# Kernel optimization log

Hardware: AMD Instinct MI355X
Metric: run time of the kernel (lower is better)

Reference implementation:

```python
import jax, jax.numpy as jnp
import numpy as np

B, S, D, H = 2, 2048, 2048, 16
HD = D // H  # head dim = 128

def setup_inputs() -> dict:
    key = jax.random.key(0)
    ks = jax.random.split(key, 5)
    x = jax.random.normal(ks[0], (B, S, D), dtype=jnp.float32)
    # causal mask: True means block that position (per docstring)
    mask = jnp.triu(jnp.ones((S, S), dtype=bool), k=1)
    scale = 1.0 / np.sqrt(D)
    Wq = jax.random.normal(ks[1], (D, D), dtype=jnp.float32) * scale
    Wk = jax.random.normal(ks[2], (D, D), dtype=jnp.float32) * scale
    Wv = jax.random.normal(ks[3], (D, D), dtype=jnp.float32) * scale
    Wo = jax.random.normal(ks[4], (D, D), dtype=jnp.float32) * scale
    return {"x": x, "mask": mask, "Wq": Wq, "Wk": Wk, "Wv": Wv, "Wo": Wo}

def _split_heads(t):
    b, s, _ = t.shape
    return t.reshape(b, s, H, HD).transpose(0, 2, 1, 3)  # (b, h, s, hd)

def reference(x, mask, Wq, Wk, Wv, Wo):
    # nn.Linear(bias=False): y = x @ W.T
    q = _split_heads(x @ Wq.T)
    k = _split_heads(x @ Wk.T)
    v = _split_heads(x @ Wv.T)
    scale = HD ** -0.5
    scores = jnp.einsum('bhqd,bhkd->bhqk', q, k) * scale  # (b,h,s,s)
    scores = jnp.where(mask[None, None, :, :], -jnp.inf, scores)
    weights = jax.nn.softmax(scores, axis=-1)  # dropout is identity at eval
    out = jnp.einsum('bhqk,bhkd->bhqd', weights, v)
    out = out.transpose(0, 2, 1, 3).reshape(x.shape[0], x.shape[1], D)
    return out @ Wo.T
```

## Files before the change

kernel.cpp:

```cpp
#include <hip/hip_runtime.h>
#include <hip/hip_bf16.h>

typedef __bf16 bf16x8 __attribute__((ext_vector_type(8)));
typedef float f32x4 __attribute__((ext_vector_type(4)));
typedef unsigned short ushort8v __attribute__((ext_vector_type(8)));

__device__ __forceinline__ unsigned short f2bf(float f) {
    unsigned int u = __float_as_uint(f);
    u = (u + 0x7fffu + ((u >> 16) & 1u)) >> 16;
    return (unsigned short)u;
}

__device__ __forceinline__ f32x4 mfma16(bf16x8 a, bf16x8 b, f32x4 c) {
    return __builtin_amdgcn_mfma_f32_16x16x32_bf16(a, b, c, 0, 0, 0);
}

__device__ __forceinline__ void store_c(unsigned short* p, float v) { *p = f2bf(v); }
__device__ __forceinline__ void store_c(float* p, float v) { *p = v; }

__global__ __launch_bounds__(256) void cast_f32_bf16(const float* __restrict__ in,
                                                     unsigned short* __restrict__ out,
                                                     int n4) {
    int i = blockIdx.x * blockDim.x + threadIdx.x;
    if (i < n4) {
        float4 f = ((const float4*)in)[i];
        ushort4 u;
        u.x = f2bf(f.x); u.y = f2bf(f.y); u.z = f2bf(f.z); u.w = f2bf(f.w);
        ((ushort4*)out)[i] = u;
    }
}

__global__ __launch_bounds__(256) void transpose_v(const unsigned short* __restrict__ v,
                                                   unsigned short* __restrict__ vt) {
    __shared__ unsigned short t[64][65];
    const int tid = threadIdx.x;
    const int s0 = blockIdx.x * 64;
    const int d0 = blockIdx.y * 64;
    const int bh = blockIdx.z;
    const int b = bh >> 4, h = bh & 15;

#pragma unroll
    for (int i = 0; i < 2; ++i) {
        int idx = i * 256 + tid;
        int r = idx >> 3, c8 = (idx & 7) * 8;
        ushort8v d = *(const ushort8v*)(v + ((size_t)(b * 2048 + s0 + r)) * 2048 + h * 128 + d0 + c8);
#pragma unroll
        for (int j = 0; j < 8; ++j) t[r][c8 + j] = d[j];
    }
    __syncthreads();
#pragma unroll
    for (int i = 0; i < 2; ++i) {
        int idx = i * 256 + tid;
        int dr = idx >> 3, sc8 = (idx & 7) * 8;
        ushort8v o;
#pragma unroll
        for (int j = 0; j < 8; ++j) o[j] = t[sc8 + j][dr];
        *(ushort8v*)(vt + ((size_t)(bh * 128 + d0 + dr)) * 2048 + s0 + sc8) = o;
    }
}

__device__ __forceinline__ void stage_tile(const unsigned short* __restrict__ A,
                                           const unsigned short* __restrict__ B,
                                           char* lAslot, char* lBslot,
                                           int row0, int col0, int kt, int K,
                                           int tid, int w) {
#pragma unroll
    for (int j = 0; j < 2; ++j) {
        int ci = j * 512 + tid;
        int r = ci >> 2, p = ci & 3;
        int c = p ^ ((r >> 1) & 3);
        size_t goff = ((size_t)(row0 + r) * K + kt + c * 8) * 2;
        __builtin_amdgcn_global_load_lds(
            (__attribute__((address_space(1))) void*)(void*)((const char*)A + goff),
            (__attribute__((address_space(3))) void*)(lAslot + (j * 512 + w * 64) * 16),
            16, 0, 0);
    }
    {
        int ci = tid;
        int r = ci >> 2, p = ci & 3;
        int c = p ^ ((r >> 1) & 3);
        size_t goff = ((size_t)(col0 + r) * K + kt + c * 8) * 2;
        __builtin_amdgcn_global_load_lds(
            (__attribute__((address_space(1))) void*)(void*)((const char*)B + goff),
            (__attribute__((address_space(3))) void*)(lBslot + (w * 64) * 16),
            16, 0, 0);
    }
}

template <typename OUT_T>
__global__ __launch_bounds__(512) void gemm_bt2(const unsigned short* __restrict__ A,
                                                const unsigned short* __restrict__ B,
                                                OUT_T* __restrict__ C,
                                                int M, int N, int K) {
    __shared__ __align__(16) unsigned short lA[3][256 * 32];
    __shared__ __align__(16) unsigned short lB[3][128 * 32];

    const int tid = threadIdx.x;
    const int w = tid >> 6, lane = tid & 63;
    const int wm = w >> 2, wn = w & 3;
    const int lane16 = lane & 15, g = lane >> 4;
    const int row0 = blockIdx.y * 256, col0 = blockIdx.x * 128;
    const int NT = K >> 5;

    f32x4 acc[8][2] = {};

    stage_tile(A, B, (char*)lA[0], (char*)lB[0], row0, col0, 0, K, tid, w);
    stage_tile(A, B, (char*)lA[1], (char*)lB[1], row0, col0, 32, K, tid, w);
    stage_tile(A, B, (char*)lA[2], (char*)lB[2], row0, col0, 64, K, tid, w);

    int s = 0;
#pragma unroll 1
    for (int t = 0; t < NT; ++t) {
        if (t + 2 < NT)      asm volatile("s_waitcnt vmcnt(6)" ::: "memory");
        else if (t + 1 < NT) asm volatile("s_waitcnt vmcnt(3)" ::: "memory");
        else                 asm volatile("s_waitcnt vmcnt(0)" ::: "memory");
        __builtin_amdgcn_s_barrier();
        asm volatile("" ::: "memory");

        bf16x8 aF[8], bF[2];
#pragma unroll
        for (int mf = 0; mf < 8; ++mf) {
            int r = wm * 128 + mf * 16 + lane16;
            aF[mf] = *(const bf16x8*)&lA[s][r * 32 + (g ^ ((r >> 1) & 3)) * 8];
        }
#pragma unroll
        for (int nf = 0; nf < 2; ++nf) {
            int r = wn * 32 + nf * 16 + lane16;
            bF[nf] = *(const bf16x8*)&lB[s][r * 32 + (g ^ ((r >> 1) & 3)) * 8];
        }
        __builtin_amdgcn_s_setprio(1);
#pragma unroll
        for (int mf = 0; mf < 8; ++mf)
#pragma unroll
            for (int nf = 0; nf < 2; ++nf)
                acc[mf][nf] = mfma16(aF[mf], bF[nf], acc[mf][nf]);
        __builtin_amdgcn_s_setprio(0);

        asm volatile("" ::: "memory");
        __builtin_amdgcn_s_barrier();
        asm volatile("" ::: "memory");

        if (t + 3 < NT)
            stage_tile(A, B, (char*)lA[s], (char*)lB[s], row0, col0, (t + 3) * 32, K, tid, w);
        s = (s == 2) ? 0 : s + 1;
    }

#pragma unroll
    for (int mf = 0; mf < 8; ++mf) {
        int r0 = row0 + wm * 128 + mf * 16 + g * 4;
#pragma unroll
        for (int nf = 0; nf < 2; ++nf) {
            int c = col0 + wn * 32 + nf * 16 + lane16;
#pragma unroll
            for (int r = 0; r < 4; ++r)
                store_c(&C[(size_t)(r0 + r) * N + c], acc[mf][nf][r]);
        }
    }
}

__global__ __launch_bounds__(256) void attn_causal(const unsigned short* __restrict__ Q,
                                                   const unsigned short* __restrict__ K,
                                                   const unsigned short* __restrict__ VT,
                                                   unsigned short* __restrict__ O) {
    __shared__ __align__(16) unsigned short lK[64 * 128];
    __shared__ __align__(16) unsigned short lVt[128 * 64];
    __shared__ __align__(16) unsigned short lP[4][16 * 80];

    const int tid = threadIdx.x, w = tid >> 6, lane = tid & 63;
    const int lane16 = lane & 15, g = lane >> 4;
    const int bh = blockIdx.y;
    const int b = bh >> 4, h = bh & 15;
    const size_t rowBase = (size_t)b * 2048;
    const int hoff = h * 128;
    const float scale = 0.08838834764831845f;

    for (int pass = 0; pass < 2; ++pass) {
        const int qt = pass ? (31 - (int)blockIdx.x) : (int)blockIdx.x;
        const int qt0 = qt * 64;
        const int qr0 = qt0 + w * 16;

        bf16x8 qa[4];
        {
            const unsigned short* qp = Q + (rowBase + qr0 + lane16) * 2048 + hoff;
#pragma unroll
            for (int kk = 0; kk < 4; ++kk)
                qa[kk] = *(const bf16x8*)(qp + kk * 32 + g * 8);
        }

        float m_r[4], l_r[4];
        f32x4 accO[8];
#pragma unroll
        for (int r = 0; r < 4; ++r) { m_r[r] = -1e30f; l_r[r] = 0.f; }
#pragma unroll
        for (int f = 0; f < 8; ++f) accO[f] = f32x4{0.f, 0.f, 0.f, 0.f};

        const int nt = qt + 1;

        for (int t = 0; t < nt; ++t) {
            const int kv0 = t * 64;
            __syncthreads();
#pragma unroll
            for (int i = 0; i < 4; ++i) {
                int ci = (w * 4 + i) * 64 + lane;
                int krow = ci >> 4;
                int kcolb = ((ci & 15) ^ (krow & 7)) * 16;
                size_t goff = ((rowBase + kv0 + krow) * 2048 + hoff) * 2 + kcolb;
                __builtin_amdgcn_global_load_lds(
                    (__attribute__((address_space(1))) void*)(void*)((const char*)K + goff),
                    (__attribute__((address_space(3))) void*)((char*)lK + (w * 4 + i) * 1024),
                    16, 0, 0);
            }
#pragma unroll
            for (int i = 0; i < 4; ++i) {
                int ci = (w * 4 + i) * 64 + lane;
                int drow = ci >> 3;
                int slot = (ci & 7) ^ (drow & 7);
                size_t goff = ((size_t)(bh * 128 + drow) * 2048 + kv0 + slot * 8) * 2;
                __builtin_amdgcn_global_load_lds(
                    (__attribute__((address_space(1))) void*)(void*)((const char*)VT + goff),
                    (__attribute__((address_space(3))) void*)((char*)lVt + (w * 4 + i) * 1024),
                    16, 0, 0);
            }
            __syncthreads();

            float p[4][4];
#pragma unroll
            for (int n = 0; n < 4; ++n) {
                f32x4 sc = {0.f, 0.f, 0.f, 0.f};
                int row = n * 16 + lane16;
#pragma unroll
                for (int kk = 0; kk < 4; ++kk) {
                    int sw = (kk * 4 + g) ^ (row & 7);
                    bf16x8 kb = *(const bf16x8*)&lK[row * 128 + sw * 8];
                    sc = mfma16(qa[kk], kb, sc);
                }
#pragma unroll
                for (int r = 0; r < 4; ++r) p[n][r] = sc[r] * scale;
            }
            if (t == nt - 1) {
#pragma unroll
                for (int n = 0; n < 4; ++n)
#pragma unroll
                    for (int r = 0; r < 4; ++r) {
                        int qi = qr0 + g * 4 + r, ki = kv0 + n * 16 + lane16;
                        if (ki > qi) p[n][r] = -1e30f;
                    }
            }
#pragma unroll
            for (int r = 0; r < 4; ++r) {
                float rm = fmaxf(fmaxf(p[0][r], p[1][r]), fmaxf(p[2][r], p[3][r]));
#pragma unroll
                for (int off = 1; off < 16; off <<= 1)
                    rm = fmaxf(rm, __shfl_xor(rm, off, 64));
                float mn = fmaxf(m_r[r], rm);
                float fac = __expf(m_r[r] - mn);
                float rs = 0.f;
#pragma unroll
                for (int n = 0; n < 4; ++n) { p[n][r] = __expf(p[n][r] - mn); rs += p[n][r]; }
#pragma unroll
                for (int off = 1; off < 16; off <<= 1)
                    rs += __shfl_xor(rs, off, 64);
                l_r[r] = l_r[r] * fac + rs;
                m_r[r] = mn;
#pragma unroll
                for (int f = 0; f < 8; ++f) accO[f][r] *= fac;
            }
#pragma unroll
            for (int n = 0; n < 4; ++n)
#pragma unroll
                for (int r = 0; r < 4; ++r)
                    lP[w][(g * 4 + r) * 80 + n * 16 + lane16] = f2bf(p[n][r]);
            asm volatile("s_waitcnt lgkmcnt(0)" ::: "memory");
#pragma unroll
            for (int kk2 = 0; kk2 < 2; ++kk2) {
                bf16x8 pa = *(const bf16x8*)&lP[w][lane16 * 80 + kk2 * 32 + g * 8];
#pragma unroll
                for (int f = 0; f < 8; ++f) {
                    int row = f * 16 + lane16;
                    int slot = (kk2 * 4 + g) ^ (row & 7);
                    bf16x8 vb = *(const bf16x8*)&lVt[row * 64 + slot * 8];
                    accO[f] = mfma16(pa, vb, accO[f]);
                }
            }
        }

#pragma unroll
        for (int f = 0; f < 8; ++f)
#pragma unroll
            for (int r = 0; r < 4; ++r) {
                float ov = accO[f][r] / l_r[r];
                O[(rowBase + qr0 + g * 4 + r) * 2048 + hoff + f * 16 + lane16] = f2bf(ov);
            }
    }
}

extern "C" void kernel_launch(void* const* d_in, const int* in_sizes, int n_in,
                              void* d_out, int out_size, void* d_ws, size_t ws_size,
                              hipStream_t stream) {
    const float* x  = (const float*)d_in[0];
    const float* Wq = (const float*)d_in[2];
    const float* Wk = (const float*)d_in[3];
    const float* Wv = (const float*)d_in[4];
    const float* Wo = (const float*)d_in[5];
    float* out = (float*)d_out;

    char* ws = (char*)d_ws;
    unsigned short* xb = (unsigned short*)(ws);
    unsigned short* q  = (unsigned short*)(ws + (size_t)(16u << 20));
    unsigned short* k  = (unsigned short*)(ws + (size_t)(32u << 20));
    unsigned short* v  = (unsigned short*)(ws + (size_t)(48u << 20));
    unsigned short* wb = (unsigned short*)(ws + (size_t)(64u << 20));
    unsigned short* vt = xb;
    unsigned short* o  = v;

    const int M = 4096, D = 2048;
    dim3 gg(D / 128, M / 256);

    cast_f32_bf16<<<(M * D / 4) / 256, 256, 0, stream>>>(x, xb, M * D / 4);

    cast_f32_bf16<<<(D * D / 4) / 256, 256, 0, stream>>>(Wq, wb, D * D / 4);
    gemm_bt2<unsigned short><<<gg, 512, 0, stream>>>(xb, wb, q, M, D, D);
    cast_f32_bf16<<<(D * D / 4) / 256, 256, 0, stream>>>(Wk, wb, D * D / 4);
    gemm_bt2<unsigned short><<<gg, 512, 0, stream>>>(xb, wb, k, M, D, D);
    cast_f32_bf16<<<(D * D / 4) / 256, 256, 0, stream>>>(Wv, wb, D * D / 4);
    gemm_bt2<unsigned short><<<gg, 512, 0, stream>>>(xb, wb, v, M, D, D);

    transpose_v<<<dim3(32, 2, 32), 256, 0, stream>>>(v, vt);

    attn_causal<<<dim3(16, 32), 256, 0, stream>>>(q, k, vt, o);

    cast_f32_bf16<<<(D * D / 4) / 256, 256, 0, stream>>>(Wo, wb, D * D / 4);
    gemm_bt2<float><<<gg, 512, 0, stream>>>(o, wb, out, M, D, D);
}
```

Baseline: 487.8 us.

## Deepen GEMM K-tile to 64 and use square 64x64 per-wave tiles

The bf16 GEMM now stages 64-wide K slices instead of 32, using a new XOR swizzle over 8 chunks and triple-buffered LDS of 144KB. The 8 waves are rearranged as 4x2, so each wave computes a 64x64 block with a 4x4 MFMA grid, where before it computed 128x32. This lowers LDS fragment reads per MFMA and halves the number of barriers per K. The cost is much higher LDS use, which limits occupancy to one block per CU and may hurt latency hiding.

```diff
diff --git a/kernel.cpp b/kernel.cpp
--- a/kernel.cpp
+++ b/kernel.cpp
@@ -59,98 +59,102 @@
     }
 }
 
-__device__ __forceinline__ void stage_tile(const unsigned short* __restrict__ A,
-                                           const unsigned short* __restrict__ B,
-                                           char* lAslot, char* lBslot,
-                                           int row0, int col0, int kt, int K,
-                                           int tid, int w) {
-#pragma unroll
-    for (int j = 0; j < 2; ++j) {
+__device__ __forceinline__ void stage3(const unsigned short* __restrict__ A,
+                                       const unsigned short* __restrict__ B,
+                                       char* lAslot, char* lBslot,
+                                       int row0, int col0, int kt, int K,
+                                       int tid, int w) {
+#pragma unroll
+    for (int j = 0; j < 4; ++j) {
         int ci = j * 512 + tid;
-        int r = ci >> 2, p = ci & 3;
-        int c = p ^ ((r >> 1) & 3);
+        int r = ci >> 3, p = ci & 7;
+        int c = p ^ (r & 7);
         size_t goff = ((size_t)(row0 + r) * K + kt + c * 8) * 2;
         __builtin_amdgcn_global_load_lds(
             (__attribute__((address_space(1))) void*)(void*)((const char*)A + goff),
             (__attribute__((address_space(3))) void*)(lAslot + (j * 512 + w * 64) * 16),
             16, 0, 0);
     }
-    {
-        int ci = tid;
-        int r = ci >> 2, p = ci & 3;
-        int c = p ^ ((r >> 1) & 3);
+#pragma unroll
+    for (int j = 0; j < 2; ++j) {
+        int ci = j * 512 + tid;
+        int r = ci >> 3, p = ci & 7;
+        int c = p ^ (r & 7);
         size_t goff = ((size_t)(col0 + r) * K + kt + c * 8) * 2;
         __builtin_amdgcn_global_load_lds(
             (__attribute__((address_space(1))) void*)(void*)((const char*)B + goff),
-            (__attribute__((address_space(3))) void*)(lBslot + (w * 64) * 16),
+            (__attribute__((address_space(3))) void*)(lBslot + (j * 512 + w * 64) * 16),
             16, 0, 0);
     }
 }
 
 template <typename OUT_T>
-__global__ __launch_bounds__(512) void gemm_bt2(const unsigned short* __restrict__ A,
+__global__ __launch_bounds__(512) void gemm_bt3(const unsigned short* __restrict__ A,
                                                 const unsigned short* __restrict__ B,
                                                 OUT_T* __restrict__ C,
                                                 int M, int N, int K) {
-    __shared__ __align__(16) unsigned short lA[3][256 * 32];
-    __shared__ __align__(16) unsigned short lB[3][128 * 32];
+    __shared__ __align__(16) unsigned short lA[3][256 * 64];
+    __shared__ __align__(16) unsigned short lB[3][128 * 64];
 
     const int tid = threadIdx.x;
     const int w = tid >> 6, lane = tid & 63;
-    const int wm = w >> 2, wn = w & 3;
+    const int wm = w >> 1, wn = w & 1;
     const int lane16 = lane & 15, g = lane >> 4;
     const int row0 = blockIdx.y * 256, col0 = blockIdx.x * 128;
-    const int NT = K >> 5;
-
-    f32x4 acc[8][2] = {};
-
-    stage_tile(A, B, (char*)lA[0], (char*)lB[0], row0, col0, 0, K, tid, w);
-    stage_tile(A, B, (char*)lA[1], (char*)lB[1], row0, col0, 32, K, tid, w);
-    stage_tile(A, B, (char*)lA[2], (char*)lB[2], row0, col0, 64, K, tid, w);
+    const int NT = K >> 6;
+
+    f32x4 acc[4][4] = {};
+
+    stage3(A, B, (char*)lA[0], (char*)lB[0], row0, col0, 0,   K, tid, w);
+    stage3(A, B, (char*)lA[1], (char*)lB[1], row0, col0, 64,  K, tid, w);
+    stage3(A, B, (char*)lA[2], (char*)lB[2], row0, col0, 128, K, tid, w);
 
     int s = 0;
 #pragma unroll 1
     for (int t = 0; t < NT; ++t) {
-        if (t + 2 < NT)      asm volatile("s_waitcnt vmcnt(6)" ::: "memory");
-        else if (t + 1 < NT) asm volatile("s_waitcnt vmcnt(3)" ::: "memory");
+        if (t + 2 < NT)      asm volatile("s_waitcnt vmcnt(12)" ::: "memory");
+        else if (t + 1 < NT) asm volatile("s_waitcnt vmcnt(6)" ::: "memory");
         else                 asm volatile("s_waitcnt vmcnt(0)" ::: "memory");
         __builtin_amdgcn_s_barrier();
         asm volatile("" ::: "memory");
 
-        bf16x8 aF[8], bF[2];
-#pragma unroll
-        for (int mf = 0; mf < 8; ++mf) {
-            int r = wm * 128 + mf * 16 + lane16;
-            aF[mf] = *(const bf16x8*)&lA[s][r * 32 + (g ^ ((r >> 1) & 3)) * 8];
+#pragma unroll
+        for (int kk = 0; kk < 2; ++kk) {
+            bf16x8 aF[4], bF[4];
+#pragma unroll
+            for (int f = 0; f < 4; ++f) {
+                int r = wm * 64 + f * 16 + lane16;
+                aF[f] = *(const bf16x8*)&lA[s][r * 64 + ((kk * 4 + g) ^ (r & 7)) * 8];
+            }
+#pragma unroll
+            for (int f = 0; f < 4; ++f) {
+                int r = wn * 64 + f * 16 + lane16;
+                bF[f] = *(const bf16x8*)&lB[s][r * 64 + ((kk * 4 + g) ^ (r & 7)) * 8];
+            }
+            __builtin_amdgcn_s_setprio(1);
+#pragma unroll
+            for (int mf = 0; mf < 4; ++mf)
+#pragma unroll
+                for (int nf = 0; nf < 4; ++nf)
+                    acc[mf][nf] = mfma16(aF[mf], bF[nf], acc[mf][nf]);
+            __builtin_amdgcn_s_setprio(0);
         }
-#pragma unroll
-        for (int nf = 0; nf < 2; ++nf) {
-            int r = wn * 32 + nf * 16 + lane16;
-            bF[nf] = *(const bf16x8*)&lB[s][r * 32 + (g ^ ((r >> 1) & 3)) * 8];
-        }
-        __builtin_amdgcn_s_setprio(1);
-#pragma unroll
-        for (int mf = 0; mf < 8; ++mf)
-#pragma unroll
-            for (int nf = 0; nf < 2; ++nf)
-                acc[mf][nf] = mfma16(aF[mf], bF[nf], acc[mf][nf]);
-        __builtin_amdgcn_s_setprio(0);
 
         asm volatile("" ::: "memory");
         __builtin_amdgcn_s_barrier();
         asm volatile("" ::: "memory");
 
         if (t + 3 < NT)
-            stage_tile(A, B, (char*)lA[s], (char*)lB[s], row0, col0, (t + 3) * 32, K, tid, w);
+            stage3(A, B, (char*)lA[s], (char*)lB[s], row0, col0, (t + 3) * 64, K, tid, w);
         s = (s == 2) ? 0 : s + 1;
     }
 
 #pragma unroll
-    for (int mf = 0; mf < 8; ++mf) {
-        int r0 = row0 + wm * 128 + mf * 16 + g * 4;
-#pragma unroll
-        for (int nf = 0; nf < 2; ++nf) {
-            int c = col0 + wn * 32 + nf * 16 + lane16;
+    for (int mf = 0; mf < 4; ++mf) {
+        int r0 = row0 + wm * 64 + mf * 16 + g * 4;
+#pragma unroll
+        for (int nf = 0; nf < 4; ++nf) {
+            int c = col0 + wn * 64 + nf * 16 + lane16;
 #pragma unroll
             for (int r = 0; r < 4; ++r)
                 store_c(&C[(size_t)(r0 + r) * N + c], acc[mf][nf][r]);
@@ -319,16 +323,16 @@
     cast_f32_bf16<<<(M * D / 4) / 256, 256, 0, stream>>>(x, xb, M * D / 4);
 
     cast_f32_bf16<<<(D * D / 4) / 256, 256, 0, stream>>>(Wq, wb, D * D / 4);
-    gemm_bt2<unsigned short><<<gg, 512, 0, stream>>>(xb, wb, q, M, D, D);
+    gemm_bt3<unsigned short><<<gg, 512, 0, stream>>>(xb, wb, q, M, D, D);
     cast_f32_bf16<<<(D * D / 4) / 256, 256, 0, stream>>>(Wk, wb, D * D / 4);
-    gemm_bt2<unsigned short><<<gg, 512, 0, stream>>>(xb, wb, k, M, D, D);
+    gemm_bt3<unsigned short><<<gg, 512, 0, stream>>>(xb, wb, k, M, D, D);
     cast_f32_bf16<<<(D * D / 4) / 256, 256, 0, stream>>>(Wv, wb, D * D / 4);
-    gemm_bt2<unsigned short><<<gg, 512, 0, stream>>>(xb, wb, v, M, D, D);
+    gemm_bt3<unsigned short><<<gg, 512, 0, stream>>>(xb, wb, v, M, D, D);
 
     transpose_v<<<dim3(32, 2, 32), 256, 0, stream>>>(v, vt);
 
     attn_causal<<<dim3(16, 32), 256, 0, stream>>>(q, k, vt, o);
 
     cast_f32_bf16<<<(D * D / 4) / 256, 256, 0, stream>>>(Wo, wb, D * D / 4);
-    gemm_bt2<float><<<gg, 512, 0, stream>>>(o, wb, out, M, D, D);
-}
+    gemm_bt3<float><<<gg, 512, 0, stream>>>(o, wb, out, M, D, D);
+}
```

After: 445.6 us. 1.09x faster.
